# Kernel tuning notes

Hardware: AMD Instinct MI355X
Metric: run time of the kernel (lower is better)

The kernel has to match this reference:

```python
import jax, jax.numpy as jnp
import numpy as np

DIM = 256
N_EMBED = 8192
BETA = 0.25


def setup_inputs() -> dict:
    key = jax.random.key(0)
    k1, k2, k3, k4 = jax.random.split(key, 4)
    inp = {
        "input": jax.random.normal(k1, (16, 1024, DIM), dtype=jnp.float32),
        # nn.Embedding weight init: normal(0, dim**-0.5)
        "embed_weight": jax.random.normal(k2, (N_EMBED, DIM), dtype=jnp.float32) * (DIM ** -0.5),
        # nn.Linear(dim, dim): weight [out, in], bias [out]
        "proj_w": jax.random.normal(k3, (DIM, DIM), dtype=jnp.float32) * (DIM ** -0.5),
        "proj_b": jax.random.normal(k4, (DIM,), dtype=jnp.float32) * 0.01,
    }
    return inp


def reference(input, embed_weight, proj_w, proj_b):
    flatten = input.reshape(-1, DIM)                      # [N, d]
    # projected codebook: Linear(embedding.weight)
    quant_codebook = embed_weight @ proj_w.T + proj_b     # [K, d]
    d = (jnp.sum(flatten ** 2, axis=1, keepdims=True)
         + jnp.sum(quant_codebook ** 2, axis=1)
         - 2.0 * jnp.einsum('nd,kd->nk', flatten, quant_codebook))  # [N, K]
    min_encoding_indices = jnp.argmin(d, axis=1)          # [N]
    z_quantize = quant_codebook[min_encoding_indices].reshape(input.shape)
    sg = jax.lax.stop_gradient
    diff = jnp.mean((sg(z_quantize) - input) ** 2)
    commit_loss = jnp.mean((z_quantize - sg(input)) ** 2)
    diff = diff + BETA * commit_loss                      # legacy=True branch
    # straight-through estimator
    z_quantize = input + sg(z_quantize - input)
    return (z_quantize, diff, min_encoding_indices)
```

## Files before the change

### kernel.cpp

```cpp
#include <hip/hip_runtime.h>

#define DIMD   256
#define NTOK   16384
#define NCODE  8192
#define NELEM  (NTOK * DIMD)

#define BM 128
#define BK 128
#define BD 32
#define PAD 4
#define LDS_STRIDE (BM + PAD)

#define SPLITS_B 4
#define CODES_PER_WAVE (NCODE / SPLITS_B / 4)
#define NGROUPS (CODES_PER_WAVE / 16)
#define MARGIN 0.5f
#define EBUF_CAP 1024

typedef float floatx4 __attribute__((ext_vector_type(4)));
typedef short short8  __attribute__((ext_vector_type(8)));

__device__ __forceinline__ unsigned short f2bf(float f) {
    unsigned u = __float_as_uint(f);
    unsigned r = (u + 0x7FFFu + ((u >> 16) & 1u)) >> 16;
    return (unsigned short)r;
}

__device__ __forceinline__ unsigned fkey(float f) {
    unsigned u = __float_as_uint(f);
    return (u & 0x80000000u) ? ~u : (u | 0x80000000u);
}
__device__ __forceinline__ float funkey(unsigned k) {
    unsigned u = (k & 0x80000000u) ? (k & 0x7FFFFFFFu) : ~k;
    return __uint_as_float(u);
}

__device__ __forceinline__ size_t cb2_idx(int row, int col) {
    return ((size_t)((row >> 4) * 8 + (col >> 5))) * 512
         + (size_t)((((col >> 3) & 3) * 16 + (row & 15)) * 8 + (col & 7));
}

__global__ __launch_bounds__(256, 3)
void project_kernel(const float* __restrict__ E, const float* __restrict__ W,
                    const float* __restrict__ bias, float* __restrict__ C,
                    unsigned short* __restrict__ Cb2)
{
    __shared__ float smem[2 * BD * LDS_STRIDE];
    float* As = smem;
    float* Bs = smem + BD * LDS_STRIDE;

    const int tid = threadIdx.x;
    const int tx  = tid & 15;
    const int ty  = tid >> 4;
    const int m0  = blockIdx.x * BM;
    const int j0  = blockIdx.y * BK;

    const int srow = tid >> 3;
    const int scol = (tid & 7) * 4;

    float acc[8][8];
#pragma unroll
    for (int i = 0; i < 8; ++i)
#pragma unroll
        for (int j = 0; j < 8; ++j) acc[i][j] = 0.f;

    for (int dc = 0; dc < DIMD / BD; ++dc) {
        const int d0 = dc * BD;
        __syncthreads();
#pragma unroll
        for (int rr = 0; rr < 4; ++rr) {
            const int r = srow + rr * 32;
            float4 av = *(const float4*)&E[(size_t)(m0 + r) * DIMD + d0 + scol];
            As[(scol + 0) * LDS_STRIDE + r] = av.x;
            As[(scol + 1) * LDS_STRIDE + r] = av.y;
            As[(scol + 2) * LDS_STRIDE + r] = av.z;
            As[(scol + 3) * LDS_STRIDE + r] = av.w;
            float4 bv = *(const float4*)&W[(size_t)(j0 + r) * DIMD + d0 + scol];
            Bs[(scol + 0) * LDS_STRIDE + r] = bv.x;
            Bs[(scol + 1) * LDS_STRIDE + r] = bv.y;
            Bs[(scol + 2) * LDS_STRIDE + r] = bv.z;
            Bs[(scol + 3) * LDS_STRIDE + r] = bv.w;
        }
        __syncthreads();
#pragma unroll 4
        for (int d = 0; d < BD; ++d) {
            float4 a0 = *(float4*)&As[d * LDS_STRIDE + ty * 4];
            float4 a1 = *(float4*)&As[d * LDS_STRIDE + 64 + ty * 4];
            float4 b0 = *(float4*)&Bs[d * LDS_STRIDE + tx * 4];
            float4 b1 = *(float4*)&Bs[d * LDS_STRIDE + 64 + tx * 4];
            float a[8] = {a0.x, a0.y, a0.z, a0.w, a1.x, a1.y, a1.z, a1.w};
            float b[8] = {b0.x, b0.y, b0.z, b0.w, b1.x, b1.y, b1.z, b1.w};
#pragma unroll
            for (int i = 0; i < 8; ++i)
#pragma unroll
                for (int j = 0; j < 8; ++j) acc[i][j] = fmaf(a[i], b[j], acc[i][j]);
        }
    }

    float4 bja = *(const float4*)&bias[j0 + tx * 4];
    float4 bjb = *(const float4*)&bias[j0 + 64 + tx * 4];
#pragma unroll
    for (int i = 0; i < 8; ++i) {
        const int mloc = (i < 4) ? (ty * 4 + i) : (64 + ty * 4 + (i - 4));
        const int row  = m0 + mloc;
        const size_t rbase = (size_t)row * DIMD;
        float o[8] = {acc[i][0] + bja.x, acc[i][1] + bja.y, acc[i][2] + bja.z, acc[i][3] + bja.w,
                      acc[i][4] + bjb.x, acc[i][5] + bjb.y, acc[i][6] + bjb.z, acc[i][7] + bjb.w};
        *(float4*)&C[rbase + j0 + tx * 4]      = *(float4*)&o[0];
        *(float4*)&C[rbase + j0 + 64 + tx * 4] = *(float4*)&o[4];
        ushort4 h0 = {f2bf(o[0]), f2bf(o[1]), f2bf(o[2]), f2bf(o[3])};
        ushort4 h1 = {f2bf(o[4]), f2bf(o[5]), f2bf(o[6]), f2bf(o[7])};
        *(ushort4*)&Cb2[cb2_idx(row, j0 + tx * 4)]      = h0;
        *(ushort4*)&Cb2[cb2_idx(row, j0 + 64 + tx * 4)] = h1;
    }
}

__global__ void convx_kernel(const float* __restrict__ X, float* __restrict__ xnorm,
                             unsigned short* __restrict__ Xb)
{
    const int wave = threadIdx.x >> 6;
    const int lane = threadIdx.x & 63;
    const int row  = blockIdx.x * 4 + wave;
    float4 v = *(const float4*)&X[(size_t)row * DIMD + lane * 4];
    ushort4 h = {f2bf(v.x), f2bf(v.y), f2bf(v.z), f2bf(v.w)};
    *(ushort4*)&Xb[(size_t)row * DIMD + lane * 4] = h;
    float s = v.x * v.x + v.y * v.y + v.z * v.z + v.w * v.w;
#pragma unroll
    for (int off = 1; off < 64; off <<= 1) s += __shfl_xor(s, off);
    if (lane == 0) xnorm[row] = s;
}

__global__ void cnorm_kernel(const float* __restrict__ A, float* __restrict__ out)
{
    const int wave = threadIdx.x >> 6;
    const int lane = threadIdx.x & 63;
    const int row  = blockIdx.x * 4 + wave;
    float4 v = *(const float4*)&A[(size_t)row * DIMD + lane * 4];
    float s = v.x * v.x + v.y * v.y + v.z * v.z + v.w * v.w;
#pragma unroll
    for (int off = 1; off < 64; off <<= 1) s += __shfl_xor(s, off);
    if (lane == 0) out[row] = s;
}

__global__ __launch_bounds__(256, 2)
void dist_min_kernel(const unsigned short* __restrict__ Xb,
                     const unsigned short* __restrict__ Cb2,
                     const float* __restrict__ cnorm,
                     unsigned* __restrict__ minkey)
{
    __shared__ float wmin[4][64];

    const int tid  = threadIdx.x;
    const int lane = tid & 63;
    const int wv   = tid >> 6;
    const int l15  = lane & 15;
    const int quad = lane >> 4;
    const int tok0 = blockIdx.x * 64;
    const int cbase = blockIdx.y * (NCODE / SPLITS_B) + wv * CODES_PER_WAVE;

    short8 a[4][8];
#pragma unroll
    for (int i = 0; i < 4; ++i) {
        const unsigned short* ap = Xb + (size_t)(tok0 + i * 16 + l15) * DIMD + quad * 8;
#pragma unroll
        for (int ks = 0; ks < 8; ++ks)
            a[i][ks] = *(const short8*)(ap + ks * 32);
    }

    float runv[16];
#pragma unroll
    for (int s = 0; s < 16; ++s) runv[s] = 3.4e38f;

    const unsigned short* bp0 = Cb2 + (size_t)cbase * DIMD + lane * 8;

    short8 breg[2][8];
    float  cnr[2];
#pragma unroll
    for (int ks = 0; ks < 8; ++ks) breg[0][ks] = *(const short8*)(bp0 + ks * 512);
    cnr[0] = cnorm[cbase + l15];

    auto group_body = [&](int g, short8 (&bc)[8], short8 (&bn)[8],
                          float cnc, float& cnn) {
        if (g + 1 < NGROUPS) {
            const unsigned short* bpn = bp0 + (size_t)(g + 1) * 4096;
#pragma unroll
            for (int ks = 0; ks < 8; ++ks) bn[ks] = *(const short8*)(bpn + ks * 512);
            cnn = cnorm[cbase + (g + 1) * 16 + l15];
        }

        floatx4 acc[4];
#pragma unroll
        for (int i = 0; i < 4; ++i) acc[i] = (floatx4){0.f, 0.f, 0.f, 0.f};
#pragma unroll
        for (int ks = 0; ks < 8; ++ks)
#pragma unroll
            for (int i = 0; i < 4; ++i)
                acc[i] = __builtin_amdgcn_mfma_f32_16x16x32_bf16(a[i][ks], bc[ks], acc[i], 0, 0, 0);

#pragma unroll
        for (int i = 0; i < 4; ++i)
#pragma unroll
            for (int r = 0; r < 4; ++r)
                runv[i * 4 + r] = fminf(runv[i * 4 + r], fmaf(-2.f, acc[i][r], cnc));
    };

    for (int gg = 0; gg < NGROUPS; gg += 2) {
        group_body(gg,     breg[0], breg[1], cnr[0], cnr[1]);
        group_body(gg + 1, breg[1], breg[0], cnr[1], cnr[0]);
    }

#pragma unroll
    for (int s = 0; s < 16; ++s) {
        float m = runv[s];
#pragma unroll
        for (int off = 1; off < 16; off <<= 1) m = fminf(m, __shfl_xor(m, off));
        runv[s] = m;
    }
    if (l15 == 0) {
#pragma unroll
        for (int i = 0; i < 4; ++i)
#pragma unroll
            for (int r = 0; r < 4; ++r)
                wmin[wv][i * 16 + quad * 4 + r] = runv[i * 4 + r];
    }
    __syncthreads();
    if (tid < 64) {
        const float bm = fminf(fminf(wmin[0][tid], wmin[1][tid]),
                               fminf(wmin[2][tid], wmin[3][tid]));
        atomicMin(&minkey[tok0 + tid], fkey(bm));
    }
}

__global__ __launch_bounds__(256, 2)
void dist_emit_kernel(const unsigned short* __restrict__ Xb,
                      const unsigned short* __restrict__ Cb2,
                      const float* __restrict__ cnorm,
                      const unsigned* __restrict__ minkey,
                      unsigned* __restrict__ list, unsigned* __restrict__ count,
                      unsigned cap)
{
    __shared__ float tokthr[64];
    __shared__ unsigned ebuf[EBUF_CAP];
    __shared__ unsigned ecnt, gbase;

    const int tid  = threadIdx.x;
    const int lane = tid & 63;
    const int wv   = tid >> 6;
    const int l15  = lane & 15;
    const int quad = lane >> 4;
    const int tok0 = blockIdx.x * 64;
    const int cbase = blockIdx.y * (NCODE / SPLITS_B) + wv * CODES_PER_WAVE;

    if (tid == 0) ecnt = 0;
    if (tid < 64) tokthr[tid] = funkey(minkey[tok0 + tid]) + MARGIN;
    __syncthreads();

    short8 a[4][8];
#pragma unroll
    for (int i = 0; i < 4; ++i) {
        const unsigned short* ap = Xb + (size_t)(tok0 + i * 16 + l15) * DIMD + quad * 8;
#pragma unroll
        for (int ks = 0; ks < 8; ++ks)
            a[i][ks] = *(const short8*)(ap + ks * 32);
    }

    float thr[16];
#pragma unroll
    for (int i = 0; i < 4; ++i)
#pragma unroll
        for (int r = 0; r < 4; ++r)
            thr[i * 4 + r] = tokthr[i * 16 + quad * 4 + r];

    const unsigned short* bp0 = Cb2 + (size_t)cbase * DIMD + lane * 8;

    short8 breg[2][8];
    float  cnr[2];
#pragma unroll
    for (int ks = 0; ks < 8; ++ks) breg[0][ks] = *(const short8*)(bp0 + ks * 512);
    cnr[0] = cnorm[cbase + l15];

    auto group_body = [&](int g, short8 (&bc)[8], short8 (&bn)[8],
                          float cnc, float& cnn) {
        const int code0 = cbase + g * 16;
        if (g + 1 < NGROUPS) {
            const unsigned short* bpn = bp0 + (size_t)(g + 1) * 4096;
#pragma unroll
            for (int ks = 0; ks < 8; ++ks) bn[ks] = *(const short8*)(bpn + ks * 512);
            cnn = cnorm[code0 + 16 + l15];
        }

        floatx4 acc[4];
#pragma unroll
        for (int i = 0; i < 4; ++i) acc[i] = (floatx4){0.f, 0.f, 0.f, 0.f};
#pragma unroll
        for (int ks = 0; ks < 8; ++ks)
#pragma unroll
            for (int i = 0; i < 4; ++i)
                acc[i] = __builtin_amdgcn_mfma_f32_16x16x32_bf16(a[i][ks], bc[ks], acc[i], 0, 0, 0);

        unsigned mask = 0;
#pragma unroll
        for (int i = 0; i < 4; ++i)
#pragma unroll
            for (int r = 0; r < 4; ++r) {
                const float dd = fmaf(-2.f, acc[i][r], cnc);
                if (dd < thr[i * 4 + r]) mask |= (1u << (i * 4 + r));
            }

        if (__any(mask != 0)) {
            if (mask) {
                unsigned pos = atomicAdd(&ecnt, (unsigned)__popc(mask));
#pragma unroll
                for (int i = 0; i < 4; ++i)
#pragma unroll
                    for (int r = 0; r < 4; ++r) {
                        const int s = i * 4 + r;
                        if (mask & (1u << s)) {
                            const unsigned token = tok0 + i * 16 + quad * 4 + r;
                            const unsigned entry = (token << 13) | (unsigned)(code0 + l15);
                            if (pos < EBUF_CAP) ebuf[pos] = entry;
                            else { unsigned gp = atomicAdd(count, 1u); if (gp < cap) list[gp] = entry; }
                            ++pos;
                        }
                    }
            }
        }
    };

    for (int gg = 0; gg < NGROUPS; gg += 2) {
        group_body(gg,     breg[0], breg[1], cnr[0], cnr[1]);
        group_body(gg + 1, breg[1], breg[0], cnr[1], cnr[0]);
    }

    __syncthreads();
    const unsigned n = (ecnt < EBUF_CAP) ? ecnt : EBUF_CAP;
    if (tid == 0) gbase = atomicAdd(count, n);
    __syncthreads();
    const unsigned gb = gbase;
    for (unsigned i = tid; i < n; i += 256) {
        const unsigned p = gb + i;
        if (p < cap) list[p] = ebuf[i];
    }
}

__global__ __launch_bounds__(256)
void rescore_kernel(const float* __restrict__ X, const float* __restrict__ C,
                    const float* __restrict__ xnorm, const float* __restrict__ cnorm,
                    const unsigned* __restrict__ list, const unsigned* __restrict__ count,
                    unsigned cap, unsigned long long* __restrict__ fin)
{
    const int lane = threadIdx.x & 63;
    const int g16  = lane & 15;
    const int sub  = lane >> 4;
    const int gid  = ((blockIdx.x * 256 + threadIdx.x) >> 6) * 4 + sub;
    const int ng   = ((gridDim.x * 256) >> 6) * 4;
    unsigned n = *count; if (n > cap) n = cap;

    for (unsigned c = gid; c < n; c += ng) {
        const unsigned e = list[c];
        const unsigned tok = e >> 13, code = e & 8191u;
        const float* xr = &X[(size_t)tok * DIMD];
        const float* cr = &C[(size_t)code * DIMD];
        float dot = 0.f;
#pragma unroll
        for (int r = 0; r < 4; ++r) {
            float4 x4 = *(const float4*)&xr[r * 64 + g16 * 4];
            float4 c4 = *(const float4*)&cr[r * 64 + g16 * 4];
            dot = fmaf(x4.x, c4.x, dot);
            dot = fmaf(x4.y, c4.y, dot);
            dot = fmaf(x4.z, c4.z, dot);
            dot = fmaf(x4.w, c4.w, dot);
        }
#pragma unroll
        for (int d = 1; d < 16; d <<= 1) dot += __shfl_xor(dot, d);
        if (g16 == 0) {
            const float dd = xnorm[tok] + cnorm[code] - 2.f * dot;
            const unsigned long long p =
                ((unsigned long long)__float_as_uint(dd) << 32) | code;
            atomicMin(&fin[tok], p);
        }
    }
}

__global__ __launch_bounds__(256)
void finalize_kernel(const float* __restrict__ X, const float* __restrict__ C,
                     const unsigned long long* __restrict__ fin,
                     float* __restrict__ out)
{
    __shared__ float part[4];
    const int lane = threadIdx.x & 63;
    const int wv   = threadIdx.x >> 6;
    const int t0   = blockIdx.x * 64;

    float local = 0.f;
    for (int it = 0; it < 16; ++it) {
        const int t = t0 + wv * 16 + it;
        const unsigned code = (unsigned)(fin[t] & 0xFFFFFFFFull);
        float4 c4 = *(const float4*)&C[(size_t)code * DIMD + lane * 4];
        float4 x4 = *(const float4*)&X[(size_t)t * DIMD + lane * 4];
        float4 w  = {c4.x - x4.x, c4.y - x4.y, c4.z - x4.z, c4.w - x4.w};
        local += w.x * w.x + w.y * w.y + w.z * w.z + w.w * w.w;
        float4 zq = {x4.x + w.x, x4.y + w.y, x4.z + w.z, x4.w + w.w};
        *(float4*)&out[(size_t)t * DIMD + lane * 4] = zq;
        if (lane == 0) out[NELEM + 1 + t] = (float)code;
    }
#pragma unroll
    for (int off = 1; off < 64; off <<= 1) local += __shfl_xor(local, off);
    if (lane == 0) part[wv] = local;
    __syncthreads();
    if (threadIdx.x == 0) {
        const float s = part[0] + part[1] + part[2] + part[3];
        atomicAdd(&out[NELEM], s * (1.25f / (float)NELEM));
    }
}

extern "C" void kernel_launch(void* const* d_in, const int* in_sizes, int n_in,
                              void* d_out, int out_size, void* d_ws, size_t ws_size,
                              hipStream_t stream)
{
    const float* X = (const float*)d_in[0];
    const float* E = (const float*)d_in[1];
    const float* W = (const float*)d_in[2];
    const float* b = (const float*)d_in[3];
    float* out = (float*)d_out;

    char* w = (char*)d_ws;
    float* C            = (float*)w;           w += (size_t)NCODE * DIMD * 4;
    unsigned short* Xb  = (unsigned short*)w;  w += (size_t)NTOK * DIMD * 2;
    unsigned short* Cb2 = (unsigned short*)w;  w += (size_t)NCODE * DIMD * 2;
    float* xnorm        = (float*)w;           w += (size_t)NTOK * 4;
    float* cnorm        = (float*)w;           w += (size_t)NCODE * 4;
    unsigned long long* fin = (unsigned long long*)w; w += (size_t)NTOK * 8;
    unsigned* minkey    = (unsigned*)w;        w += (size_t)NTOK * 4;
    unsigned* cnt       = (unsigned*)w;        w += 256;
    unsigned* list      = (unsigned*)w;

    size_t used = (size_t)(w - (char*)d_ws);
    size_t avail = (ws_size > used) ? (ws_size - used) / 4 : 0;
    unsigned cap = (unsigned)((avail > 16777216u) ? 16777216u : avail);

    hipMemsetAsync(cnt, 0, 4, stream);
    hipMemsetAsync(fin, 0xFF, (size_t)NTOK * 8, stream);
    hipMemsetAsync(minkey, 0xFF, (size_t)NTOK * 4, stream);
    hipMemsetAsync(out + NELEM, 0, 4, stream);

    project_kernel<<<dim3(NCODE / BM, DIMD / BK), 256, 0, stream>>>(E, W, b, C, Cb2);
    convx_kernel<<<NTOK / 4, 256, 0, stream>>>(X, xnorm, Xb);
    cnorm_kernel<<<NCODE / 4, 256, 0, stream>>>(C, cnorm);
    dist_min_kernel<<<dim3(NTOK / 64, SPLITS_B), 256, 0, stream>>>(
        Xb, Cb2, cnorm, minkey);
    dist_emit_kernel<<<dim3(NTOK / 64, SPLITS_B), 256, 0, stream>>>(
        Xb, Cb2, cnorm, minkey, list, cnt, cap);
    rescore_kernel<<<1024, 256, 0, stream>>>(X, C, xnorm, cnorm, list, cnt, cap, fin);
    finalize_kernel<<<NTOK / 64, 256, 0, stream>>>(X, C, fin, out);
}
```

Measured before the change: 289.4 us.

## Fuse codebook norm into projection, split MFMA accumulators, merge memsets

Computes the squared norms of the projected codebook inside the projection kernel's epilogue. Each block reduces its partial row sums through shared memory and adds them into cnorm with atomics, which removes the separate cnorm kernel launch and its reread of C. The distance kernels now use two independent MFMA accumulator chains (even and odd k-steps), summed at the end, to shorten the dependency chain. The workspace is reordered so cnorm and cnt, and fin and minkey, are each cleared with one memset. This adds float atomics with a nondeterministic summation order and more accumulator registers.

New measurement: 310.1 us. +7.2%, slower.

```diff
diff --git a/kernel.cpp b/kernel.cpp
--- a/kernel.cpp
+++ b/kernel.cpp
@@ -43,7 +43,7 @@
 __global__ __launch_bounds__(256, 3)
 void project_kernel(const float* __restrict__ E, const float* __restrict__ W,
                     const float* __restrict__ bias, float* __restrict__ C,
-                    unsigned short* __restrict__ Cb2)
+                    unsigned short* __restrict__ Cb2, float* __restrict__ cnorm)
 {
     __shared__ float smem[2 * BD * LDS_STRIDE];
     float* As = smem;
@@ -97,6 +97,9 @@
         }
     }
 
+    __syncthreads();
+    float* red = smem;
+
     float4 bja = *(const float4*)&bias[j0 + tx * 4];
     float4 bjb = *(const float4*)&bias[j0 + 64 + tx * 4];
 #pragma unroll
@@ -112,6 +115,17 @@
         ushort4 h1 = {f2bf(o[4]), f2bf(o[5]), f2bf(o[6]), f2bf(o[7])};
         *(ushort4*)&Cb2[cb2_idx(row, j0 + tx * 4)]      = h0;
         *(ushort4*)&Cb2[cb2_idx(row, j0 + 64 + tx * 4)] = h1;
+        float p = 0.f;
+#pragma unroll
+        for (int j = 0; j < 8; ++j) p = fmaf(o[j], o[j], p);
+        red[mloc * 16 + tx] = p;
+    }
+    __syncthreads();
+    if (tid < 128) {
+        float s = 0.f;
+#pragma unroll
+        for (int k = 0; k < 16; ++k) s += red[tid * 16 + k];
+        atomicAdd(&cnorm[m0 + tid], s);
     }
 }
 
@@ -130,18 +144,6 @@
     if (lane == 0) xnorm[row] = s;
 }
 
-__global__ void cnorm_kernel(const float* __restrict__ A, float* __restrict__ out)
-{
-    const int wave = threadIdx.x >> 6;
-    const int lane = threadIdx.x & 63;
-    const int row  = blockIdx.x * 4 + wave;
-    float4 v = *(const float4*)&A[(size_t)row * DIMD + lane * 4];
-    float s = v.x * v.x + v.y * v.y + v.z * v.z + v.w * v.w;
-#pragma unroll
-    for (int off = 1; off < 64; off <<= 1) s += __shfl_xor(s, off);
-    if (lane == 0) out[row] = s;
-}
-
 __global__ __launch_bounds__(256, 2)
 void dist_min_kernel(const unsigned short* __restrict__ Xb,
                      const unsigned short* __restrict__ Cb2,
@@ -188,20 +190,28 @@
             cnn = cnorm[cbase + (g + 1) * 16 + l15];
         }
 
-        floatx4 acc[4];
-#pragma unroll
-        for (int i = 0; i < 4; ++i) acc[i] = (floatx4){0.f, 0.f, 0.f, 0.f};
-#pragma unroll
-        for (int ks = 0; ks < 8; ++ks)
+        floatx4 alo[4], ahi[4];
+#pragma unroll
+        for (int i = 0; i < 4; ++i) {
+            alo[i] = (floatx4){0.f, 0.f, 0.f, 0.f};
+            ahi[i] = (floatx4){0.f, 0.f, 0.f, 0.f};
+        }
+#pragma unroll
+        for (int ks = 0; ks < 8; ks += 2) {
 #pragma unroll
             for (int i = 0; i < 4; ++i)
-                acc[i] = __builtin_amdgcn_mfma_f32_16x16x32_bf16(a[i][ks], bc[ks], acc[i], 0, 0, 0);
+                alo[i] = __builtin_amdgcn_mfma_f32_16x16x32_bf16(a[i][ks], bc[ks], alo[i], 0, 0, 0);
+#pragma unroll
+            for (int i = 0; i < 4; ++i)
+                ahi[i] = __builtin_amdgcn_mfma_f32_16x16x32_bf16(a[i][ks + 1], bc[ks + 1], ahi[i], 0, 0, 0);
+        }
 
 #pragma unroll
         for (int i = 0; i < 4; ++i)
 #pragma unroll
             for (int r = 0; r < 4; ++r)
-                runv[i * 4 + r] = fminf(runv[i * 4 + r], fmaf(-2.f, acc[i][r], cnc));
+                runv[i * 4 + r] = fminf(runv[i * 4 + r],
+                                        fmaf(-2.f, alo[i][r] + ahi[i][r], cnc));
     };
 
     for (int gg = 0; gg < NGROUPS; gg += 2) {
@@ -289,22 +299,31 @@
             cnn = cnorm[code0 + 16 + l15];
         }
 
-        floatx4 acc[4];
-#pragma unroll
-        for (int i = 0; i < 4; ++i) acc[i] = (floatx4){0.f, 0.f, 0.f, 0.f};
-#pragma unroll
-        for (int ks = 0; ks < 8; ++ks)
+        floatx4 alo[4], ahi[4];
+#pragma unroll
+        for (int i = 0; i < 4; ++i) {
+            alo[i] = (floatx4){0.f, 0.f, 0.f, 0.f};
+            ahi[i] = (floatx4){0.f, 0.f, 0.f, 0.f};
+        }
+#pragma unroll
+        for (int ks = 0; ks < 8; ks += 2) {
 #pragma unroll
             for (int i = 0; i < 4; ++i)
-                acc[i] = __builtin_amdgcn_mfma_f32_16x16x32_bf16(a[i][ks], bc[ks], acc[i], 0, 0, 0);
+                alo[i] = __builtin_amdgcn_mfma_f32_16x16x32_bf16(a[i][ks], bc[ks], alo[i], 0, 0, 0);
+#pragma unroll
+            for (int i = 0; i < 4; ++i)
+                ahi[i] = __builtin_amdgcn_mfma_f32_16x16x32_bf16(a[i][ks + 1], bc[ks + 1], ahi[i], 0, 0, 0);
+        }
 
         unsigned mask = 0;
+        float dv[16];
 #pragma unroll
         for (int i = 0; i < 4; ++i)
 #pragma unroll
             for (int r = 0; r < 4; ++r) {
-                const float dd = fmaf(-2.f, acc[i][r], cnc);
-                if (dd < thr[i * 4 + r]) mask |= (1u << (i * 4 + r));
+                const int s = i * 4 + r;
+                dv[s] = fmaf(-2.f, alo[i][r] + ahi[i][r], cnc);
+                if (dv[s] < thr[s]) mask |= (1u << s);
             }
 
         if (__any(mask != 0)) {
@@ -430,23 +449,21 @@
     unsigned short* Cb2 = (unsigned short*)w;  w += (size_t)NCODE * DIMD * 2;
     float* xnorm        = (float*)w;           w += (size_t)NTOK * 4;
     float* cnorm        = (float*)w;           w += (size_t)NCODE * 4;
+    unsigned* cnt       = (unsigned*)w;        w += 256;
     unsigned long long* fin = (unsigned long long*)w; w += (size_t)NTOK * 8;
     unsigned* minkey    = (unsigned*)w;        w += (size_t)NTOK * 4;
-    unsigned* cnt       = (unsigned*)w;        w += 256;
     unsigned* list      = (unsigned*)w;
 
     size_t used = (size_t)(w - (char*)d_ws);
     size_t avail = (ws_size > used) ? (ws_size - used) / 4 : 0;
     unsigned cap = (unsigned)((avail > 16777216u) ? 16777216u : avail);
 
-    hipMemsetAsync(cnt, 0, 4, stream);
-    hipMemsetAsync(fin, 0xFF, (size_t)NTOK * 8, stream);
-    hipMemsetAsync(minkey, 0xFF, (size_t)NTOK * 4, stream);
+    hipMemsetAsync(cnorm, 0, (size_t)NCODE * 4 + 256, stream);
+    hipMemsetAsync(fin, 0xFF, (size_t)NTOK * 8 + (size_t)NTOK * 4, stream);
     hipMemsetAsync(out + NELEM, 0, 4, stream);
 
-    project_kernel<<<dim3(NCODE / BM, DIMD / BK), 256, 0, stream>>>(E, W, b, C, Cb2);
+    project_kernel<<<dim3(NCODE / BM, DIMD / BK), 256, 0, stream>>>(E, W, b, C, Cb2, cnorm);
     convx_kernel<<<NTOK / 4, 256, 0, stream>>>(X, xnorm, Xb);
-    cnorm_kernel<<<NCODE / 4, 256, 0, stream>>>(C, cnorm);
     dist_min_kernel<<<dim3(NTOK / 64, SPLITS_B), 256, 0, stream>>>(
         Xb, Cb2, cnorm, minkey);
     dist_emit_kernel<<<dim3(NTOK / 64, SPLITS_B), 256, 0, stream>>>(
```

## Fuse codebook norm into projection, halve dist_min token tile, merge memsets

Applied to the files above, without the earlier changes.

Codebook squared norms are now computed in the projection epilogue through an LDS row reduction plus an atomicAdd per row-half, so the separate cnorm kernel is gone. dist_min_kernel now handles 32 tokens per block instead of 64, doubling the grid and cutting A-fragment registers. That raises occupancy but reloads the codebook twice as often. The workspace is reordered so that cnorm/cnt and fin/minkey are each cleared by one memset, removing launches.

Measured after the change: 306.3 us. +5.8%, slower.

```diff
diff --git a/kernel.cpp b/kernel.cpp
--- a/kernel.cpp
+++ b/kernel.cpp
@@ -43,7 +43,7 @@
 __global__ __launch_bounds__(256, 3)
 void project_kernel(const float* __restrict__ E, const float* __restrict__ W,
                     const float* __restrict__ bias, float* __restrict__ C,
-                    unsigned short* __restrict__ Cb2)
+                    unsigned short* __restrict__ Cb2, float* __restrict__ cnorm)
 {
     __shared__ float smem[2 * BD * LDS_STRIDE];
     float* As = smem;
@@ -97,6 +97,9 @@
         }
     }
 
+    __syncthreads();
+    float* red = smem;
+
     float4 bja = *(const float4*)&bias[j0 + tx * 4];
     float4 bjb = *(const float4*)&bias[j0 + 64 + tx * 4];
 #pragma unroll
@@ -112,6 +115,17 @@
         ushort4 h1 = {f2bf(o[4]), f2bf(o[5]), f2bf(o[6]), f2bf(o[7])};
         *(ushort4*)&Cb2[cb2_idx(row, j0 + tx * 4)]      = h0;
         *(ushort4*)&Cb2[cb2_idx(row, j0 + 64 + tx * 4)] = h1;
+        float p = 0.f;
+#pragma unroll
+        for (int j = 0; j < 8; ++j) p = fmaf(o[j], o[j], p);
+        red[mloc * 16 + tx] = p;
+    }
+    __syncthreads();
+    if (tid < 128) {
+        float s = 0.f;
+#pragma unroll
+        for (int k = 0; k < 16; ++k) s += red[tid * 16 + k];
+        atomicAdd(&cnorm[m0 + tid], s);
     }
 }
 
@@ -130,46 +144,34 @@
     if (lane == 0) xnorm[row] = s;
 }
 
-__global__ void cnorm_kernel(const float* __restrict__ A, float* __restrict__ out)
-{
-    const int wave = threadIdx.x >> 6;
-    const int lane = threadIdx.x & 63;
-    const int row  = blockIdx.x * 4 + wave;
-    float4 v = *(const float4*)&A[(size_t)row * DIMD + lane * 4];
-    float s = v.x * v.x + v.y * v.y + v.z * v.z + v.w * v.w;
-#pragma unroll
-    for (int off = 1; off < 64; off <<= 1) s += __shfl_xor(s, off);
-    if (lane == 0) out[row] = s;
-}
-
 __global__ __launch_bounds__(256, 2)
 void dist_min_kernel(const unsigned short* __restrict__ Xb,
                      const unsigned short* __restrict__ Cb2,
                      const float* __restrict__ cnorm,
                      unsigned* __restrict__ minkey)
 {
-    __shared__ float wmin[4][64];
+    __shared__ float wmin[4][32];
 
     const int tid  = threadIdx.x;
     const int lane = tid & 63;
     const int wv   = tid >> 6;
     const int l15  = lane & 15;
     const int quad = lane >> 4;
-    const int tok0 = blockIdx.x * 64;
+    const int tok0 = blockIdx.x * 32;
     const int cbase = blockIdx.y * (NCODE / SPLITS_B) + wv * CODES_PER_WAVE;
 
-    short8 a[4][8];
-#pragma unroll
-    for (int i = 0; i < 4; ++i) {
+    short8 a[2][8];
+#pragma unroll
+    for (int i = 0; i < 2; ++i) {
         const unsigned short* ap = Xb + (size_t)(tok0 + i * 16 + l15) * DIMD + quad * 8;
 #pragma unroll
         for (int ks = 0; ks < 8; ++ks)
             a[i][ks] = *(const short8*)(ap + ks * 32);
     }
 
-    float runv[16];
-#pragma unroll
-    for (int s = 0; s < 16; ++s) runv[s] = 3.4e38f;
+    float runv[8];
+#pragma unroll
+    for (int s = 0; s < 8; ++s) runv[s] = 3.4e38f;
 
     const unsigned short* bp0 = Cb2 + (size_t)cbase * DIMD + lane * 8;
 
@@ -188,17 +190,17 @@
             cnn = cnorm[cbase + (g + 1) * 16 + l15];
         }
 
-        floatx4 acc[4];
-#pragma unroll
-        for (int i = 0; i < 4; ++i) acc[i] = (floatx4){0.f, 0.f, 0.f, 0.f};
+        floatx4 acc[2];
+#pragma unroll
+        for (int i = 0; i < 2; ++i) acc[i] = (floatx4){0.f, 0.f, 0.f, 0.f};
 #pragma unroll
         for (int ks = 0; ks < 8; ++ks)
 #pragma unroll
-            for (int i = 0; i < 4; ++i)
+            for (int i = 0; i < 2; ++i)
                 acc[i] = __builtin_amdgcn_mfma_f32_16x16x32_bf16(a[i][ks], bc[ks], acc[i], 0, 0, 0);
 
 #pragma unroll
-        for (int i = 0; i < 4; ++i)
+        for (int i = 0; i < 2; ++i)
 #pragma unroll
             for (int r = 0; r < 4; ++r)
                 runv[i * 4 + r] = fminf(runv[i * 4 + r], fmaf(-2.f, acc[i][r], cnc));
@@ -210,7 +212,7 @@
     }
 
 #pragma unroll
-    for (int s = 0; s < 16; ++s) {
+    for (int s = 0; s < 8; ++s) {
         float m = runv[s];
 #pragma unroll
         for (int off = 1; off < 16; off <<= 1) m = fminf(m, __shfl_xor(m, off));
@@ -218,13 +220,13 @@
     }
     if (l15 == 0) {
 #pragma unroll
-        for (int i = 0; i < 4; ++i)
+        for (int i = 0; i < 2; ++i)
 #pragma unroll
             for (int r = 0; r < 4; ++r)
                 wmin[wv][i * 16 + quad * 4 + r] = runv[i * 4 + r];
     }
     __syncthreads();
-    if (tid < 64) {
+    if (tid < 32) {
         const float bm = fminf(fminf(wmin[0][tid], wmin[1][tid]),
                                fminf(wmin[2][tid], wmin[3][tid]));
         atomicMin(&minkey[tok0 + tid], fkey(bm));
@@ -430,24 +432,22 @@
     unsigned short* Cb2 = (unsigned short*)w;  w += (size_t)NCODE * DIMD * 2;
     float* xnorm        = (float*)w;           w += (size_t)NTOK * 4;
     float* cnorm        = (float*)w;           w += (size_t)NCODE * 4;
+    unsigned* cnt       = (unsigned*)w;        w += 256;
     unsigned long long* fin = (unsigned long long*)w; w += (size_t)NTOK * 8;
     unsigned* minkey    = (unsigned*)w;        w += (size_t)NTOK * 4;
-    unsigned* cnt       = (unsigned*)w;        w += 256;
     unsigned* list      = (unsigned*)w;
 
     size_t used = (size_t)(w - (char*)d_ws);
     size_t avail = (ws_size > used) ? (ws_size - used) / 4 : 0;
     unsigned cap = (unsigned)((avail > 16777216u) ? 16777216u : avail);
 
-    hipMemsetAsync(cnt, 0, 4, stream);
-    hipMemsetAsync(fin, 0xFF, (size_t)NTOK * 8, stream);
-    hipMemsetAsync(minkey, 0xFF, (size_t)NTOK * 4, stream);
+    hipMemsetAsync(cnorm, 0, (size_t)NCODE * 4 + 256, stream);
+    hipMemsetAsync(fin, 0xFF, (size_t)NTOK * 8 + (size_t)NTOK * 4, stream);
     hipMemsetAsync(out + NELEM, 0, 4, stream);
 
-    project_kernel<<<dim3(NCODE / BM, DIMD / BK), 256, 0, stream>>>(E, W, b, C, Cb2);
+    project_kernel<<<dim3(NCODE / BM, DIMD / BK), 256, 0, stream>>>(E, W, b, C, Cb2, cnorm);
     convx_kernel<<<NTOK / 4, 256, 0, stream>>>(X, xnorm, Xb);
-    cnorm_kernel<<<NCODE / 4, 256, 0, stream>>>(C, cnorm);
-    dist_min_kernel<<<dim3(NTOK / 64, SPLITS_B), 256, 0, stream>>>(
+    dist_min_kernel<<<dim3(NTOK / 32, SPLITS_B), 256, 0, stream>>>(
         Xb, Cb2, cnorm, minkey);
     dist_emit_kernel<<<dim3(NTOK / 64, SPLITS_B), 256, 0, stream>>>(
         Xb, Cb2, cnorm, minkey, list, cnt, cap);
```

## Fuse projection, token conversion, codebook norms and buffer init into one prep kernel

Applied to the files above, without the earlier changes.

Merges project_kernel, convx_kernel and cnorm_kernel into a single launch, with block-index dispatch between GEMM blocks and token-conversion blocks. The codebook norm is now computed in the projection epilogue as two partial sums, one per column half, and consumers add them. The four memset calls are replaced by writes inside the prep kernel. This removes three launches and four memsets plus a re-read of C. In exchange, every consumer does an extra load and add, and the norm is summed in a different order from before.

Result: faster. 278.2 us (-3.9%).

```diff
diff --git a/kernel.cpp b/kernel.cpp
--- a/kernel.cpp
+++ b/kernel.cpp
@@ -17,6 +17,9 @@
 #define MARGIN 0.5f
 #define EBUF_CAP 1024
 
+#define PROJ_BLOCKS ((NCODE / BM) * (DIMD / BK))
+#define CONV_BLOCKS (NTOK / 4)
+
 typedef float floatx4 __attribute__((ext_vector_type(4)));
 typedef short short8  __attribute__((ext_vector_type(8)));
 
@@ -41,19 +44,48 @@
 }
 
 __global__ __launch_bounds__(256, 3)
-void project_kernel(const float* __restrict__ E, const float* __restrict__ W,
-                    const float* __restrict__ bias, float* __restrict__ C,
-                    unsigned short* __restrict__ Cb2)
+void prep_kernel(const float* __restrict__ E, const float* __restrict__ W,
+                 const float* __restrict__ bias, float* __restrict__ C,
+                 unsigned short* __restrict__ Cb2,
+                 float* __restrict__ cnormA, float* __restrict__ cnormB,
+                 const float* __restrict__ X, float* __restrict__ xnorm,
+                 unsigned short* __restrict__ Xb,
+                 unsigned long long* __restrict__ fin,
+                 unsigned* __restrict__ minkey,
+                 unsigned* __restrict__ cnt, float* __restrict__ out)
 {
     __shared__ float smem[2 * BD * LDS_STRIDE];
+
+    const int bid = blockIdx.x;
+    const int tid = threadIdx.x;
+
+    if (bid >= PROJ_BLOCKS) {
+        const int row0 = (bid - PROJ_BLOCKS) * 4;
+        const int wave = tid >> 6;
+        const int lane = tid & 63;
+        const int row  = row0 + wave;
+        float4 v = *(const float4*)&X[(size_t)row * DIMD + lane * 4];
+        ushort4 h = {f2bf(v.x), f2bf(v.y), f2bf(v.z), f2bf(v.w)};
+        *(ushort4*)&Xb[(size_t)row * DIMD + lane * 4] = h;
+        float s = v.x * v.x + v.y * v.y + v.z * v.z + v.w * v.w;
+#pragma unroll
+        for (int off = 1; off < 64; off <<= 1) s += __shfl_xor(s, off);
+        if (lane == 0) xnorm[row] = s;
+        if (tid < 4) {
+            fin[row0 + tid]    = ~0ull;
+            minkey[row0 + tid] = ~0u;
+        }
+        if (bid == PROJ_BLOCKS && tid == 0) { *cnt = 0; out[NELEM] = 0.f; }
+        return;
+    }
+
     float* As = smem;
     float* Bs = smem + BD * LDS_STRIDE;
 
-    const int tid = threadIdx.x;
     const int tx  = tid & 15;
     const int ty  = tid >> 4;
-    const int m0  = blockIdx.x * BM;
-    const int j0  = blockIdx.y * BK;
+    const int m0  = (bid & 63) * BM;
+    const int j0  = (bid >> 6) * BK;
 
     const int srow = tid >> 3;
     const int scol = (tid & 7) * 4;
@@ -97,6 +129,9 @@
         }
     }
 
+    __syncthreads();
+    float* red = smem;
+
     float4 bja = *(const float4*)&bias[j0 + tx * 4];
     float4 bjb = *(const float4*)&bias[j0 + 64 + tx * 4];
 #pragma unroll
@@ -112,40 +147,26 @@
         ushort4 h1 = {f2bf(o[4]), f2bf(o[5]), f2bf(o[6]), f2bf(o[7])};
         *(ushort4*)&Cb2[cb2_idx(row, j0 + tx * 4)]      = h0;
         *(ushort4*)&Cb2[cb2_idx(row, j0 + 64 + tx * 4)] = h1;
-    }
-}
-
-__global__ void convx_kernel(const float* __restrict__ X, float* __restrict__ xnorm,
-                             unsigned short* __restrict__ Xb)
-{
-    const int wave = threadIdx.x >> 6;
-    const int lane = threadIdx.x & 63;
-    const int row  = blockIdx.x * 4 + wave;
-    float4 v = *(const float4*)&X[(size_t)row * DIMD + lane * 4];
-    ushort4 h = {f2bf(v.x), f2bf(v.y), f2bf(v.z), f2bf(v.w)};
-    *(ushort4*)&Xb[(size_t)row * DIMD + lane * 4] = h;
-    float s = v.x * v.x + v.y * v.y + v.z * v.z + v.w * v.w;
-#pragma unroll
-    for (int off = 1; off < 64; off <<= 1) s += __shfl_xor(s, off);
-    if (lane == 0) xnorm[row] = s;
-}
-
-__global__ void cnorm_kernel(const float* __restrict__ A, float* __restrict__ out)
-{
-    const int wave = threadIdx.x >> 6;
-    const int lane = threadIdx.x & 63;
-    const int row  = blockIdx.x * 4 + wave;
-    float4 v = *(const float4*)&A[(size_t)row * DIMD + lane * 4];
-    float s = v.x * v.x + v.y * v.y + v.z * v.z + v.w * v.w;
-#pragma unroll
-    for (int off = 1; off < 64; off <<= 1) s += __shfl_xor(s, off);
-    if (lane == 0) out[row] = s;
+        float p = 0.f;
+#pragma unroll
+        for (int j = 0; j < 8; ++j) p = fmaf(o[j], o[j], p);
+        red[mloc * 16 + tx] = p;
+    }
+    __syncthreads();
+    if (tid < 128) {
+        float s = 0.f;
+#pragma unroll
+        for (int k = 0; k < 16; ++k) s += red[tid * 16 + k];
+        float* dst = (j0 == 0) ? cnormA : cnormB;
+        dst[m0 + tid] = s;
+    }
 }
 
 __global__ __launch_bounds__(256, 2)
 void dist_min_kernel(const unsigned short* __restrict__ Xb,
                      const unsigned short* __restrict__ Cb2,
-                     const float* __restrict__ cnorm,
+                     const float* __restrict__ cnormA,
+                     const float* __restrict__ cnormB,
                      unsigned* __restrict__ minkey)
 {
     __shared__ float wmin[4][64];
@@ -177,7 +198,7 @@
     float  cnr[2];
 #pragma unroll
     for (int ks = 0; ks < 8; ++ks) breg[0][ks] = *(const short8*)(bp0 + ks * 512);
-    cnr[0] = cnorm[cbase + l15];
+    cnr[0] = cnormA[cbase + l15] + cnormB[cbase + l15];
 
     auto group_body = [&](int g, short8 (&bc)[8], short8 (&bn)[8],
                           float cnc, float& cnn) {
@@ -185,7 +206,8 @@
             const unsigned short* bpn = bp0 + (size_t)(g + 1) * 4096;
 #pragma unroll
             for (int ks = 0; ks < 8; ++ks) bn[ks] = *(const short8*)(bpn + ks * 512);
-            cnn = cnorm[cbase + (g + 1) * 16 + l15];
+            const int cnx = cbase + (g + 1) * 16 + l15;
+            cnn = cnormA[cnx] + cnormB[cnx];
         }
 
         floatx4 acc[4];
@@ -234,7 +256,8 @@
 __global__ __launch_bounds__(256, 2)
 void dist_emit_kernel(const unsigned short* __restrict__ Xb,
                       const unsigned short* __restrict__ Cb2,
-                      const float* __restrict__ cnorm,
+                      const float* __restrict__ cnormA,
+                      const float* __restrict__ cnormB,
                       const unsigned* __restrict__ minkey,
                       unsigned* __restrict__ list, unsigned* __restrict__ count,
                       unsigned cap)
@@ -277,7 +300,7 @@
     float  cnr[2];
 #pragma unroll
     for (int ks = 0; ks < 8; ++ks) breg[0][ks] = *(const short8*)(bp0 + ks * 512);
-    cnr[0] = cnorm[cbase + l15];
+    cnr[0] = cnormA[cbase + l15] + cnormB[cbase + l15];
 
     auto group_body = [&](int g, short8 (&bc)[8], short8 (&bn)[8],
                           float cnc, float& cnn) {
@@ -286,7 +309,8 @@
             const unsigned short* bpn = bp0 + (size_t)(g + 1) * 4096;
 #pragma unroll
             for (int ks = 0; ks < 8; ++ks) bn[ks] = *(const short8*)(bpn + ks * 512);
-            cnn = cnorm[code0 + 16 + l15];
+            const int cnx = code0 + 16 + l15;
+            cnn = cnormA[cnx] + cnormB[cnx];
         }
 
         floatx4 acc[4];
@@ -345,7 +369,9 @@
 
 __global__ __launch_bounds__(256)
 void rescore_kernel(const float* __restrict__ X, const float* __restrict__ C,
-                    const float* __restrict__ xnorm, const float* __restrict__ cnorm,
+                    const float* __restrict__ xnorm,
+                    const float* __restrict__ cnormA,
+                    const float* __restrict__ cnormB,
                     const unsigned* __restrict__ list, const unsigned* __restrict__ count,
                     unsigned cap, unsigned long long* __restrict__ fin)
 {
@@ -374,7 +400,7 @@
 #pragma unroll
         for (int d = 1; d < 16; d <<= 1) dot += __shfl_xor(dot, d);
         if (g16 == 0) {
-            const float dd = xnorm[tok] + cnorm[code] - 2.f * dot;
+            const float dd = xnorm[tok] + (cnormA[code] + cnormB[code]) - 2.f * dot;
             const unsigned long long p =
                 ((unsigned long long)__float_as_uint(dd) << 32) | code;
             atomicMin(&fin[tok], p);
@@ -429,28 +455,23 @@
     unsigned short* Xb  = (unsigned short*)w;  w += (size_t)NTOK * DIMD * 2;
     unsigned short* Cb2 = (unsigned short*)w;  w += (size_t)NCODE * DIMD * 2;
     float* xnorm        = (float*)w;           w += (size_t)NTOK * 4;
-    float* cnorm        = (float*)w;           w += (size_t)NCODE * 4;
+    float* cnormA       = (float*)w;           w += (size_t)NCODE * 4;
+    float* cnormB       = (float*)w;           w += (size_t)NCODE * 4;
+    unsigned* cnt       = (unsigned*)w;        w += 256;
     unsigned long long* fin = (unsigned long long*)w; w += (size_t)NTOK * 8;
     unsigned* minkey    = (unsigned*)w;        w += (size_t)NTOK * 4;
-    unsigned* cnt       = (unsigned*)w;        w += 256;
     unsigned* list      = (unsigned*)w;
 
     size_t used = (size_t)(w - (char*)d_ws);
     size_t avail = (ws_size > used) ? (ws_size - used) / 4 : 0;
     unsigned cap = (unsigned)((avail > 16777216u) ? 16777216u : avail);
 
-    hipMemsetAsync(cnt, 0, 4, stream);
-    hipMemsetAsync(fin, 0xFF, (size_t)NTOK * 8, stream);
-    hipMemsetAsync(minkey, 0xFF, (size_t)NTOK * 4, stream);
-    hipMemsetAsync(out + NELEM, 0, 4, stream);
-
-    project_kernel<<<dim3(NCODE / BM, DIMD / BK), 256, 0, stream>>>(E, W, b, C, Cb2);
-    convx_kernel<<<NTOK / 4, 256, 0, stream>>>(X, xnorm, Xb);
-    cnorm_kernel<<<NCODE / 4, 256, 0, stream>>>(C, cnorm);
+    prep_kernel<<<PROJ_BLOCKS + CONV_BLOCKS, 256, 0, stream>>>(
+        E, W, b, C, Cb2, cnormA, cnormB, X, xnorm, Xb, fin, minkey, cnt, out);
     dist_min_kernel<<<dim3(NTOK / 64, SPLITS_B), 256, 0, stream>>>(
-        Xb, Cb2, cnorm, minkey);
+        Xb, Cb2, cnormA, cnormB, minkey);
     dist_emit_kernel<<<dim3(NTOK / 64, SPLITS_B), 256, 0, stream>>>(
-        Xb, Cb2, cnorm, minkey, list, cnt, cap);
-    rescore_kernel<<<1024, 256, 0, stream>>>(X, C, xnorm, cnorm, list, cnt, cap, fin);
+        Xb, Cb2, cnormA, cnormB, minkey, list, cnt, cap);
+    rescore_kernel<<<1024, 256, 0, stream>>>(X, C, xnorm, cnormA, cnormB, list, cnt, cap, fin);
     finalize_kernel<<<NTOK / 64, 256, 0, stream>>>(X, C, fin, out);
 }
```
